# Performance work log

Hardware: AMD Instinct MI355X
Metric: run time of the kernel (lower is better)

## Reference

```python
import jax, jax.numpy as jnp
import numpy as np

N_LEVELS = 16
F = 2
LOG2_T = 19
T = 1 << LOG2_T
BASE_RES = 16.0
FINEST_RES = 512.0
N_SAMPLES = 128
NEAR, FAR = 2.0, 6.0
BOX_MIN = jnp.array([-1.5, -1.5, -1.5], jnp.float32)
BOX_MAX = jnp.array([1.5, 1.5, 1.5], jnp.float32)
GEO_FEAT = 15
OUT_CH = 4

_PRIMES = np.array([1, 2654435761, 805459861], dtype=np.uint32)
_OFFSETS = np.array([[i, j, k] for i in (0, 1) for j in (0, 1) for k in (0, 1)], dtype=np.int32)  # [8,3]
_B = np.exp((np.log(FINEST_RES) - np.log(BASE_RES)) / (N_LEVELS - 1))
_RESOLUTIONS = np.floor(BASE_RES * _B ** np.arange(N_LEVELS)).astype(np.float32)


def setup_inputs() -> dict:
    key = jax.random.key(0)
    ks = jax.random.split(key, 10)
    n_rays = 16384
    o = jax.random.uniform(ks[0], (n_rays, 3), jnp.float32, -0.5, 0.5)
    d = jax.random.normal(ks[1], (n_rays, 3), jnp.float32)
    d = d / jnp.linalg.norm(d, axis=-1, keepdims=True)
    rays = jnp.concatenate([o, d], -1)
    hash_tables = jax.random.uniform(ks[2], (N_LEVELS, T, F), jnp.float32, -1e-4, 1e-4)
    def w(k, di, do):
        return jax.random.normal(k, (di, do), jnp.float32) * (1.0 / np.sqrt(di))
    return dict(
        rays=rays,
        hash_tables=hash_tables,
        ws0=w(ks[3], 32, 64), ws1=w(ks[4], 64, 64), ws2=w(ks[5], 64, 1 + GEO_FEAT),
        wc0=w(ks[6], 16 + GEO_FEAT, 64), wc1=w(ks[7], 64, 64), wc2=w(ks[8], 64, 64), wc3=w(ks[9], 64, OUT_CH - 1),
    )


def _hash_embed(x, tables):
    """Multi-res hash grid: x [P,3] world coords, tables [L,T,F] -> ([P,L*F], keep_mask [P])."""
    xc = jnp.clip(x, BOX_MIN, BOX_MAX)
    keep = jnp.all(x == xc, axis=-1)
    offs = jnp.asarray(_OFFSETS)          # [8,3]
    primes = jnp.asarray(_PRIMES)         # uint32
    feats = []
    for l in range(N_LEVELS):
        grid = (BOX_MAX - BOX_MIN) / _RESOLUTIONS[l]
        bl = jnp.floor((xc - BOX_MIN) / grid).astype(jnp.int32)   # [P,3] bottom-left voxel index
        vmin = bl.astype(jnp.float32) * grid + BOX_MIN
        wts = (xc - vmin) / grid                                  # trilinear weights [P,3]
        corners = (bl[:, None, :] + offs[None]).astype(jnp.uint32)  # [P,8,3]
        h = (corners[..., 0] * primes[0]) ^ (corners[..., 1] * primes[1]) ^ (corners[..., 2] * primes[2])
        idx = (h & jnp.uint32(T - 1)).astype(jnp.int32)           # [P,8]
        e = tables[l][idx]                                        # [P,8,F]
        w0, w1, w2 = wts[:, 0:1], wts[:, 1:2], wts[:, 2:3]
        c00 = e[:, 0] * (1 - w0) + e[:, 4] * w0
        c01 = e[:, 1] * (1 - w0) + e[:, 5] * w0
        c10 = e[:, 2] * (1 - w0) + e[:, 6] * w0
        c11 = e[:, 3] * (1 - w0) + e[:, 7] * w0
        c0 = c00 * (1 - w1) + c10 * w1
        c1 = c01 * (1 - w1) + c11 * w1
        feats.append(c0 * (1 - w2) + c1 * w2)
    return jnp.concatenate(feats, -1), keep


def _sh_encode(d):
    """Degree-4 spherical harmonics encoding, [P,3] -> [P,16]."""
    x, y, z = d[..., 0], d[..., 1], d[..., 2]
    xx, yy, zz = x * x, y * y, z * z
    xy, yz, xz = x * y, y * z, x * z
    C0 = 0.28209479177387814
    C1 = 0.4886025119029199
    C2 = (1.0925484305920792, -1.0925484305920792, 0.31539156525252005, -1.0925484305920792, 0.5462742152960396)
    C3 = (-0.5900435899266435, 2.890611442640554, -0.4570457994644658, 0.3731763325901154,
          -0.4570457994644658, 1.445305721320277, -0.5900435899266435)
    return jnp.stack([
        jnp.full_like(x, C0),
        -C1 * y, C1 * z, -C1 * x,
        C2[0] * xy, C2[1] * yz, C2[2] * (2.0 * zz - xx - yy), C2[3] * xz, C2[4] * (xx - yy),
        C3[0] * y * (3.0 * xx - yy), C3[1] * xy * z, C3[2] * y * (4.0 * zz - xx - yy),
        C3[3] * z * (2.0 * zz - 3.0 * xx - 3.0 * yy), C3[4] * x * (4.0 * zz - xx - yy),
        C3[5] * z * (xx - yy), C3[6] * x * (xx - 3.0 * yy),
    ], axis=-1)


def _forward(rays, hash_tables, ws0, ws1, ws2, wc0, wc1, wc2, wc3):
    n_rays = rays.shape[0]
    o, d = rays[:, :3], rays[:, 3:6]
    z = jnp.linspace(NEAR, FAR, N_SAMPLES, dtype=jnp.float32)
    zvals = jnp.broadcast_to(z, (n_rays, N_SAMPLES))
    pts = o[:, None, :] + d[:, None, :] * z[None, :, None]       # [N,S,3]
    P = n_rays * N_SAMPLES
    pts_f = pts.reshape(P, 3)
    dirs_f = jnp.broadcast_to(d[:, None, :], (n_rays, N_SAMPLES, 3)).reshape(P, 3)

    enc_pts, keep = _hash_embed(pts_f, hash_tables)              # [P,32], [P]
    enc_dirs = _sh_encode(dirs_f)                                # [P,16]

    # NeRFSmall: bias-free sigma net then color net
    h = jnp.maximum(enc_pts @ ws0, 0.0)
    h = jnp.maximum(h @ ws1, 0.0)
    h = h @ ws2                                                   # [P, 1+GEO_FEAT]
    sigma, geo = h[:, 0], h[:, 1:]
    hc = jnp.concatenate([enc_dirs, geo], -1)
    hc = jnp.maximum(hc @ wc0, 0.0)
    hc = jnp.maximum(hc @ wc1, 0.0)
    hc = jnp.maximum(hc @ wc2, 0.0)
    color = hc @ wc3                                              # [P, OUT_CH-1]

    sigma = jnp.where(keep, sigma, 0.0)                           # output[~keep_mask, -1] = 0
    raw = jnp.concatenate([color, sigma[:, None]], -1).reshape(n_rays, N_SAMPLES, OUT_CH)

    # Integrator (raw2outputs)
    dists = zvals[:, 1:] - zvals[:, :-1]
    dists = jnp.concatenate([dists, jnp.full((n_rays, 1), 1e10, jnp.float32)], -1)
    dists = dists * jnp.linalg.norm(d, axis=-1, keepdims=True)
    chs = jax.nn.sigmoid(raw[..., :-1])
    alpha = 1.0 - jnp.exp(-jnp.maximum(raw[..., -1], 0.0) * dists)
    trans = jnp.cumprod(1.0 - alpha + 1e-10, axis=-1)
    trans = jnp.concatenate([jnp.ones((n_rays, 1), jnp.float32), trans[:, :-1]], -1)
    weights = alpha * trans
    chs_map = jnp.einsum('ns,nsc->nc', weights, chs)
    depth_map = jnp.sum(weights * zvals, -1)
    probs = jnp.concatenate([weights, 1.0 - jnp.sum(weights, -1, keepdims=True) + 1e-6], -1)
    p = probs / jnp.sum(probs, -1, keepdims=True)
    sparsity_loss = -jnp.sum(p * jnp.log(jnp.clip(p, 1e-37)), -1)
    return chs_map, depth_map, sparsity_loss


def reference(rays, hash_tables, ws0, ws1, ws2, wc0, wc1, wc2, wc3):
    return _forward(rays, hash_tables, ws0, ws1, ws2, wc0, wc1, wc2, wc3)
```

## Files before the change

kernel.cpp:

```cpp
#include <hip/hip_runtime.h>

#define NRAYS 16384
#define NLEV  16
#define THASH 524288
#define MAXACT 48
#define MAXPTS (NRAYS*MAXACT)
#define MBLK  512
#define MGRID 1024

__device__ __forceinline__ float zval32(int i) {
  const float step = 4.0f / 127.0f;
  return __fadd_rn(2.0f, __fmul_rn((float)i, step));
}
__device__ __forceinline__ float pcoord(float o, float d, float z) {
  return __fadd_rn(o, __fmul_rn(d, z));
}

__global__ __launch_bounds__(64)
void k_classify(const float* __restrict__ rays,
                float* __restrict__ sh,
                unsigned* __restrict__ counter,
                unsigned* __restrict__ rbase,
                unsigned* __restrict__ rn,
                unsigned* __restrict__ plist) {
  int r = blockIdx.x * 64 + threadIdx.x;
  if (r >= NRAYS) return;
  float ox = rays[6*r+0], oy = rays[6*r+1], oz = rays[6*r+2];
  float dx = rays[6*r+3], dy = rays[6*r+4], dz = rays[6*r+5];
  float x = dx, y = dy, z = dz;
  float xx = x*x, yy = y*y, zz = z*z, xy = x*y, yz = y*z, xz = x*z;
  float* shp = sh + 16*r;
  shp[0]  = 0.28209479177387814f;
  shp[1]  = -0.4886025119029199f * y;
  shp[2]  =  0.4886025119029199f * z;
  shp[3]  = -0.4886025119029199f * x;
  shp[4]  =  1.0925484305920792f * xy;
  shp[5]  = -1.0925484305920792f * yz;
  shp[6]  =  0.31539156525252005f * (2.0f*zz - xx - yy);
  shp[7]  = -1.0925484305920792f * xz;
  shp[8]  =  0.5462742152960396f * (xx - yy);
  shp[9]  = -0.5900435899266435f * y * (3.0f*xx - yy);
  shp[10] =  2.890611442640554f  * xy * z;
  shp[11] = -0.4570457994644658f * y * (4.0f*zz - xx - yy);
  shp[12] =  0.3731763325901154f * z * (2.0f*zz - 3.0f*xx - 3.0f*yy);
  shp[13] = -0.4570457994644658f * x * (4.0f*zz - xx - yy);
  shp[14] =  1.445305721320277f  * z * (xx - yy);
  shp[15] = -0.5900435899266435f * x * (xx - 3.0f*yy);
  int n = 0;
  for (int i = 0; i < 128; ++i) {
    float zi = zval32(i);
    float px = pcoord(ox, dx, zi);
    float py = pcoord(oy, dy, zi);
    float pz = pcoord(oz, dz, zi);
    bool in = (px >= -1.5f) && (px <= 1.5f) && (py >= -1.5f) && (py <= 1.5f)
           && (pz >= -1.5f) && (pz <= 1.5f);
    if (!in) break;
    ++n;
  }
  unsigned base = atomicAdd(counter, (unsigned)n);
  rbase[r] = base;
  rn[r]    = (unsigned)n;
  for (int i = 0; i < n; ++i) plist[base + i] = (unsigned)(r*128 + i);
}

template<int IN, int TOTOUT, int JC, bool RELU>
__device__ __forceinline__ void layer(const float* __restrict__ W, int jbase,
                                      const float* __restrict__ in,
                                      float* __restrict__ out, int lane) {
  float acc[JC];
#pragma unroll
  for (int j = 0; j < JC; ++j) acc[j] = 0.0f;
#pragma unroll 4
  for (int k = 0; k < IN; ++k) {
    float a = in[k*64 + lane];
    const float* Wk = W + k*TOTOUT + jbase;
#pragma unroll
    for (int j = 0; j < JC; ++j) acc[j] = fmaf(a, Wk[j], acc[j]);
  }
#pragma unroll
  for (int j = 0; j < JC; ++j)
    out[(jbase + j)*64 + lane] = RELU ? fmaxf(acc[j], 0.0f) : acc[j];
}

__global__ __launch_bounds__(MBLK)
void k_mlp(const float* __restrict__ rays,
           const float* __restrict__ tables,
           const float* __restrict__ w_s0, const float* __restrict__ w_s1,
           const float* __restrict__ w_s2, const float* __restrict__ w_c0,
           const float* __restrict__ w_c1, const float* __restrict__ w_c2,
           const float* __restrict__ w_c3,
           const float* __restrict__ sh,
           const unsigned* __restrict__ counter,
           const unsigned* __restrict__ plist,
           float4* __restrict__ results) {
  __shared__ float bufA[64*64];
  __shared__ float bufB[64*64];
  __shared__ float sig_s[64];
  __shared__ unsigned pid_s[64];
  const int t = threadIdx.x;
  const int lane = t & 63;
  const int q = __builtin_amdgcn_readfirstlane(t >> 6);
  const unsigned count = *counter;
  const unsigned ntiles = (count + 63u) >> 6;
  const float RESF[NLEV] = {16.f,20.f,25.f,32.f,40.f,50.f,64.f,80.f,
                            101.f,128.f,161.f,203.f,256.f,322.f,406.f,512.f};
  for (unsigned tile = blockIdx.x; tile < ntiles; tile += MGRID) {
    unsigned s0 = tile << 6;
    if (t < 64) {
      unsigned s = s0 + (unsigned)t;
      pid_s[t] = (s < count) ? plist[s] : 0u;
    }
    __syncthreads();
    {
      unsigned pid = pid_s[lane];
      int r = (int)(pid >> 7);
      int i = (int)(pid & 127u);
      float zi = zval32(i);
      float px = pcoord(rays[6*r+0], rays[6*r+3], zi);
      float py = pcoord(rays[6*r+1], rays[6*r+4], zi);
      float pz = pcoord(rays[6*r+2], rays[6*r+5], zi);
      float xcx = fminf(fmaxf(px, -1.5f), 1.5f);
      float xcy = fminf(fmaxf(py, -1.5f), 1.5f);
      float xcz = fminf(fmaxf(pz, -1.5f), 1.5f);
#pragma unroll
      for (int li = 0; li < 2; ++li) {
        int l = 2*q + li;
        const float grid = 3.0f / RESF[l];
        float bfx = floorf(__fdiv_rn(__fadd_rn(xcx, 1.5f), grid));
        float bfy = floorf(__fdiv_rn(__fadd_rn(xcy, 1.5f), grid));
        float bfz = floorf(__fdiv_rn(__fadd_rn(xcz, 1.5f), grid));
        float vmx = __fadd_rn(__fmul_rn(bfx, grid), -1.5f);
        float vmy = __fadd_rn(__fmul_rn(bfy, grid), -1.5f);
        float vmz = __fadd_rn(__fmul_rn(bfz, grid), -1.5f);
        float wx = __fdiv_rn(__fsub_rn(xcx, vmx), grid);
        float wy = __fdiv_rn(__fsub_rn(xcy, vmy), grid);
        float wz = __fdiv_rn(__fsub_rn(xcz, vmz), grid);
        unsigned cx0 = (unsigned)(int)bfx, cy0 = (unsigned)(int)bfy, cz0 = (unsigned)(int)bfz;
        unsigned cx1 = cx0 + 1u, cy1 = cy0 + 1u, cz1 = cz0 + 1u;
        unsigned hy0 = cy0*2654435761u, hy1 = cy1*2654435761u;
        unsigned hz0 = cz0*805459861u,  hz1 = cz1*805459861u;
        const float2* tb = (const float2*)tables + (size_t)l*THASH;
        float2 e000 = tb[(cx0^hy0^hz0)&(THASH-1)];
        float2 e001 = tb[(cx0^hy0^hz1)&(THASH-1)];
        float2 e010 = tb[(cx0^hy1^hz0)&(THASH-1)];
        float2 e011 = tb[(cx0^hy1^hz1)&(THASH-1)];
        float2 e100 = tb[(cx1^hy0^hz0)&(THASH-1)];
        float2 e101 = tb[(cx1^hy0^hz1)&(THASH-1)];
        float2 e110 = tb[(cx1^hy1^hz0)&(THASH-1)];
        float2 e111 = tb[(cx1^hy1^hz1)&(THASH-1)];
        float iwx = 1.f-wx, iwy = 1.f-wy, iwz = 1.f-wz;
        float c00a = e000.x*iwx + e100.x*wx, c00b = e000.y*iwx + e100.y*wx;
        float c01a = e001.x*iwx + e101.x*wx, c01b = e001.y*iwx + e101.y*wx;
        float c10a = e010.x*iwx + e110.x*wx, c10b = e010.y*iwx + e110.y*wx;
        float c11a = e011.x*iwx + e111.x*wx, c11b = e011.y*iwx + e111.y*wx;
        float c0a = c00a*iwy + c10a*wy, c0b = c00b*iwy + c10b*wy;
        float c1a = c01a*iwy + c11a*wy, c1b = c01b*iwy + c11b*wy;
        bufA[(2*l+0)*64 + lane] = c0a*iwz + c1a*wz;
        bufA[(2*l+1)*64 + lane] = c0b*iwz + c1b*wz;
      }
    }
    __syncthreads();
    layer<32,64,8,true >(w_s0, q*8, bufA, bufB, lane); __syncthreads();
    layer<64,64,8,true >(w_s1, q*8, bufB, bufA, lane); __syncthreads();
    layer<64,16,2,false>(w_s2, q*2, bufA, bufB, lane); __syncthreads();
    if (q == 0) sig_s[lane] = bufB[0*64 + lane];
    for (int idx = t; idx < 31*64; idx += MBLK) {
      int k = idx >> 6, p = idx & 63;
      float v;
      if (k < 16) v = sh[(pid_s[p] >> 7)*16 + k];
      else        v = bufB[(k-15)*64 + p];
      bufA[idx] = v;
    }
    __syncthreads();
    layer<31,64,8,true >(w_c0, q*8, bufA, bufB, lane); __syncthreads();
    layer<64,64,8,true >(w_c1, q*8, bufB, bufA, lane); __syncthreads();
    layer<64,64,8,true >(w_c2, q*8, bufA, bufB, lane); __syncthreads();
    if (q < 3) layer<64,3,1,false>(w_c3, q, bufB, bufA, lane);
    __syncthreads();
    if (q == 0) {
      unsigned s = s0 + (unsigned)lane;
      if (s < count) {
        float4 res;
        res.x = sig_s[lane];
        res.y = bufA[0*64 + lane];
        res.z = bufA[1*64 + lane];
        res.w = bufA[2*64 + lane];
        results[s] = res;
      }
    }
    __syncthreads();
  }
}

__global__ __launch_bounds__(64)
void k_comp(const float* __restrict__ rays,
            const unsigned* __restrict__ rbase,
            const unsigned* __restrict__ rn,
            const float4* __restrict__ results,
            float* __restrict__ out) {
  int r = blockIdx.x * 64 + threadIdx.x;
  if (r >= NRAYS) return;
  float dx = rays[6*r+3], dy = rays[6*r+4], dz = rays[6*r+5];
  float dnorm = sqrtf(dx*dx + dy*dy + dz*dz);
  int n = (int)rn[r];
  unsigned base = rbase[r];
  const float step = 4.0f/127.0f;
  const float diststep = __fmul_rn(step, dnorm);
  float S = 0.f, ch0 = 0.f, ch1 = 0.f, ch2 = 0.f, dep = 0.f, trans = 1.f;
  for (int i = 0; i < n; ++i) {
    float4 rs = results[base + i];
    float z = zval32(i);
    float sg = fmaxf(rs.x, 0.f);
    float alpha = -expm1f(-__fmul_rn(sg, diststep));
    float w = __fmul_rn(alpha, trans);
    trans = __fmul_rn(trans, __fadd_rn(__fsub_rn(1.f, alpha), 1e-10f));
    float s0 = 1.f/(1.f + expf(-rs.y));
    float s1 = 1.f/(1.f + expf(-rs.z));
    float s2 = 1.f/(1.f + expf(-rs.w));
    S += w; ch0 += w*s0; ch1 += w*s1; ch2 += w*s2; dep += w*z;
  }
  float rem  = __fadd_rn(__fsub_rn(1.f, S), 1e-6f);
  float Stot = __fadd_rn(S, rem);
  float loss = 0.f, trans2 = 1.f;
  for (int i = 0; i < n; ++i) {
    float4 rs = results[base + i];
    float sg = fmaxf(rs.x, 0.f);
    float alpha = -expm1f(-__fmul_rn(sg, diststep));
    float w = __fmul_rn(alpha, trans2);
    trans2 = __fmul_rn(trans2, __fadd_rn(__fsub_rn(1.f, alpha), 1e-10f));
    float p = __fdiv_rn(w, Stot);
    loss += p * logf(fmaxf(p, 1e-37f));
  }
  float pl = __fdiv_rn(rem, Stot);
  loss += pl * logf(fmaxf(pl, 1e-37f));
  out[3*r+0] = ch0; out[3*r+1] = ch1; out[3*r+2] = ch2;
  out[3*NRAYS + r] = dep;
  out[4*NRAYS + r] = -loss;
}

extern "C" void kernel_launch(void* const* d_in, const int* in_sizes, int n_in,
                              void* d_out, int out_size, void* d_ws, size_t ws_size,
                              hipStream_t stream) {
  const float* rays   = (const float*)d_in[0];
  const float* tables = (const float*)d_in[1];
  const float* ws0    = (const float*)d_in[2];
  const float* ws1    = (const float*)d_in[3];
  const float* ws2    = (const float*)d_in[4];
  const float* wc0    = (const float*)d_in[5];
  const float* wc1    = (const float*)d_in[6];
  const float* wc2    = (const float*)d_in[7];
  const float* wc3    = (const float*)d_in[8];

  char* ws = (char*)d_ws;
  unsigned* counter = (unsigned*)ws;
  unsigned* rbase   = (unsigned*)(ws + 256);
  unsigned* rn      = (unsigned*)(ws + 256 + 65536);
  float*    sh      = (float*)  (ws + 256 + 131072);
  float4*   results = (float4*) (ws + 1179904);
  unsigned* plist   = (unsigned*)(ws + 1179904 + (size_t)MAXPTS*16);

  hipMemsetAsync(counter, 0, 4, stream);
  k_classify<<<NRAYS/64, 64, 0, stream>>>(rays, sh, counter, rbase, rn, plist);
  k_mlp<<<MGRID, MBLK, 0, stream>>>(rays, tables, ws0, ws1, ws2,
                                    wc0, wc1, wc2, wc3, sh, counter, plist, results);
  k_comp<<<NRAYS/64, 64, 0, stream>>>(rays, rbase, rn, results, (float*)d_out);
}
```

Measured before the change: 185.4 us.

## Run MLP tile in a single wavefront per block and wave-aggregate classify atomics

The MLP kernel now uses one 64-thread wavefront per block. That wavefront computes all 16 hash levels itself and every layer with 64 accumulators per thread, so all __syncthreads barriers go away and each lane keeps a full point in registers. Classify replaces the per-thread atomicAdd with a wave prefix scan and a single atomic per wave. The trade is much higher register pressure (64 accumulators) and far fewer waves per CU, since each block still reserves 32KB of LDS. Latency hiding for the hash-table gathers is likely to get worse.

```diff
diff --git a/kernel.cpp b/kernel.cpp
--- a/kernel.cpp
+++ b/kernel.cpp
@@ -5,8 +5,7 @@
 #define THASH 524288
 #define MAXACT 48
 #define MAXPTS (NRAYS*MAXACT)
-#define MBLK  512
-#define MGRID 1024
+#define MGRID 2048
 
 __device__ __forceinline__ float zval32(int i) {
   const float step = 4.0f / 127.0f;
@@ -23,7 +22,8 @@
                 unsigned* __restrict__ rbase,
                 unsigned* __restrict__ rn,
                 unsigned* __restrict__ plist) {
-  int r = blockIdx.x * 64 + threadIdx.x;
+  int lane = threadIdx.x;
+  int r = blockIdx.x * 64 + lane;
   if (r >= NRAYS) return;
   float ox = rays[6*r+0], oy = rays[6*r+1], oz = rays[6*r+2];
   float dx = rays[6*r+3], dy = rays[6*r+4], dz = rays[6*r+5];
@@ -46,7 +46,7 @@
   shp[13] = -0.4570457994644658f * x * (4.0f*zz - xx - yy);
   shp[14] =  1.445305721320277f  * z * (xx - yy);
   shp[15] = -0.5900435899266435f * x * (xx - 3.0f*yy);
-  int n = 0;
+  unsigned n = 0;
   for (int i = 0; i < 128; ++i) {
     float zi = zval32(i);
     float px = pcoord(ox, dx, zi);
@@ -57,32 +57,43 @@
     if (!in) break;
     ++n;
   }
-  unsigned base = atomicAdd(counter, (unsigned)n);
+  unsigned pre = n;
+#pragma unroll
+  for (int d = 1; d < 64; d <<= 1) {
+    unsigned v = __shfl_up(pre, d, 64);
+    if (lane >= d) pre += v;
+  }
+  unsigned excl  = pre - n;
+  unsigned total = __shfl(pre, 63, 64);
+  unsigned base0 = 0;
+  if (lane == 0) base0 = atomicAdd(counter, total);
+  base0 = __shfl(base0, 0, 64);
+  unsigned base = base0 + excl;
   rbase[r] = base;
-  rn[r]    = (unsigned)n;
-  for (int i = 0; i < n; ++i) plist[base + i] = (unsigned)(r*128 + i);
-}
-
-template<int IN, int TOTOUT, int JC, bool RELU>
-__device__ __forceinline__ void layer(const float* __restrict__ W, int jbase,
-                                      const float* __restrict__ in,
-                                      float* __restrict__ out, int lane) {
-  float acc[JC];
-#pragma unroll
-  for (int j = 0; j < JC; ++j) acc[j] = 0.0f;
-#pragma unroll 4
+  rn[r]    = n;
+  for (unsigned i = 0; i < n; ++i) plist[base + i] = (unsigned)(r*128 + (int)i);
+}
+
+template<int IN, int TOTOUT, bool RELU>
+__device__ __forceinline__ void layerw(const float* __restrict__ W,
+                                       const float* __restrict__ in,
+                                       float* __restrict__ out, int lane) {
+  float acc[TOTOUT];
+#pragma unroll
+  for (int j = 0; j < TOTOUT; ++j) acc[j] = 0.0f;
+#pragma unroll 2
   for (int k = 0; k < IN; ++k) {
     float a = in[k*64 + lane];
-    const float* Wk = W + k*TOTOUT + jbase;
-#pragma unroll
-    for (int j = 0; j < JC; ++j) acc[j] = fmaf(a, Wk[j], acc[j]);
-  }
-#pragma unroll
-  for (int j = 0; j < JC; ++j)
-    out[(jbase + j)*64 + lane] = RELU ? fmaxf(acc[j], 0.0f) : acc[j];
-}
-
-__global__ __launch_bounds__(MBLK)
+    const float* Wk = W + k*TOTOUT;
+#pragma unroll
+    for (int j = 0; j < TOTOUT; ++j) acc[j] = fmaf(a, Wk[j], acc[j]);
+  }
+#pragma unroll
+  for (int j = 0; j < TOTOUT; ++j)
+    out[j*64 + lane] = RELU ? fmaxf(acc[j], 0.0f) : acc[j];
+}
+
+__global__ __launch_bounds__(64, 2)
 void k_mlp(const float* __restrict__ rays,
            const float* __restrict__ tables,
            const float* __restrict__ w_s0, const float* __restrict__ w_s1,
@@ -93,102 +104,86 @@
            const unsigned* __restrict__ counter,
            const unsigned* __restrict__ plist,
            float4* __restrict__ results) {
-  __shared__ float bufA[64*64];
-  __shared__ float bufB[64*64];
-  __shared__ float sig_s[64];
-  __shared__ unsigned pid_s[64];
-  const int t = threadIdx.x;
-  const int lane = t & 63;
-  const int q = __builtin_amdgcn_readfirstlane(t >> 6);
+  __shared__ float A[64*64];
+  __shared__ float B[64*64];
+  const int lane = threadIdx.x;
   const unsigned count = *counter;
   const unsigned ntiles = (count + 63u) >> 6;
   const float RESF[NLEV] = {16.f,20.f,25.f,32.f,40.f,50.f,64.f,80.f,
                             101.f,128.f,161.f,203.f,256.f,322.f,406.f,512.f};
   for (unsigned tile = blockIdx.x; tile < ntiles; tile += MGRID) {
-    unsigned s0 = tile << 6;
-    if (t < 64) {
-      unsigned s = s0 + (unsigned)t;
-      pid_s[t] = (s < count) ? plist[s] : 0u;
+    unsigned s = (tile << 6) + (unsigned)lane;
+    unsigned pid = (s < count) ? plist[s] : 0u;
+    int r = (int)(pid >> 7);
+    int i = (int)(pid & 127u);
+    float zi = zval32(i);
+    float px = pcoord(rays[6*r+0], rays[6*r+3], zi);
+    float py = pcoord(rays[6*r+1], rays[6*r+4], zi);
+    float pz = pcoord(rays[6*r+2], rays[6*r+5], zi);
+    float xcx = fminf(fmaxf(px, -1.5f), 1.5f);
+    float xcy = fminf(fmaxf(py, -1.5f), 1.5f);
+    float xcz = fminf(fmaxf(pz, -1.5f), 1.5f);
+#pragma unroll
+    for (int l = 0; l < NLEV; ++l) {
+      const float grid = 3.0f / RESF[l];
+      float bfx = floorf(__fdiv_rn(__fadd_rn(xcx, 1.5f), grid));
+      float bfy = floorf(__fdiv_rn(__fadd_rn(xcy, 1.5f), grid));
+      float bfz = floorf(__fdiv_rn(__fadd_rn(xcz, 1.5f), grid));
+      float vmx = __fadd_rn(__fmul_rn(bfx, grid), -1.5f);
+      float vmy = __fadd_rn(__fmul_rn(bfy, grid), -1.5f);
+      float vmz = __fadd_rn(__fmul_rn(bfz, grid), -1.5f);
+      float wx = __fdiv_rn(__fsub_rn(xcx, vmx), grid);
+      float wy = __fdiv_rn(__fsub_rn(xcy, vmy), grid);
+      float wz = __fdiv_rn(__fsub_rn(xcz, vmz), grid);
+      unsigned cx0 = (unsigned)(int)bfx, cy0 = (unsigned)(int)bfy, cz0 = (unsigned)(int)bfz;
+      unsigned cx1 = cx0 + 1u, cy1 = cy0 + 1u, cz1 = cz0 + 1u;
+      unsigned hy0 = cy0*2654435761u, hy1 = cy1*2654435761u;
+      unsigned hz0 = cz0*805459861u,  hz1 = cz1*805459861u;
+      const float2* tb = (const float2*)tables + (size_t)l*THASH;
+      float2 e000 = tb[(cx0^hy0^hz0)&(THASH-1)];
+      float2 e001 = tb[(cx0^hy0^hz1)&(THASH-1)];
+      float2 e010 = tb[(cx0^hy1^hz0)&(THASH-1)];
+      float2 e011 = tb[(cx0^hy1^hz1)&(THASH-1)];
+      float2 e100 = tb[(cx1^hy0^hz0)&(THASH-1)];
+      float2 e101 = tb[(cx1^hy0^hz1)&(THASH-1)];
+      float2 e110 = tb[(cx1^hy1^hz0)&(THASH-1)];
+      float2 e111 = tb[(cx1^hy1^hz1)&(THASH-1)];
+      float iwx = 1.f-wx, iwy = 1.f-wy, iwz = 1.f-wz;
+      float c00a = e000.x*iwx + e100.x*wx, c00b = e000.y*iwx + e100.y*wx;
+      float c01a = e001.x*iwx + e101.x*wx, c01b = e001.y*iwx + e101.y*wx;
+      float c10a = e010.x*iwx + e110.x*wx, c10b = e010.y*iwx + e110.y*wx;
+      float c11a = e011.x*iwx + e111.x*wx, c11b = e011.y*iwx + e111.y*wx;
+      float c0a = c00a*iwy + c10a*wy, c0b = c00b*iwy + c10b*wy;
+      float c1a = c01a*iwy + c11a*wy, c1b = c01b*iwy + c11b*wy;
+      A[(2*l+0)*64 + lane] = c0a*iwz + c1a*wz;
+      A[(2*l+1)*64 + lane] = c0b*iwz + c1b*wz;
     }
-    __syncthreads();
+    layerw<32,64,true >(w_s0, A, B, lane);
+    layerw<64,64,true >(w_s1, B, A, lane);
+    layerw<64,16,false>(w_s2, A, B, lane);
+    float sigma = B[0*64 + lane];
     {
-      unsigned pid = pid_s[lane];
-      int r = (int)(pid >> 7);
-      int i = (int)(pid & 127u);
-      float zi = zval32(i);
-      float px = pcoord(rays[6*r+0], rays[6*r+3], zi);
-      float py = pcoord(rays[6*r+1], rays[6*r+4], zi);
-      float pz = pcoord(rays[6*r+2], rays[6*r+5], zi);
-      float xcx = fminf(fmaxf(px, -1.5f), 1.5f);
-      float xcy = fminf(fmaxf(py, -1.5f), 1.5f);
-      float xcz = fminf(fmaxf(pz, -1.5f), 1.5f);
-#pragma unroll
-      for (int li = 0; li < 2; ++li) {
-        int l = 2*q + li;
-        const float grid = 3.0f / RESF[l];
-        float bfx = floorf(__fdiv_rn(__fadd_rn(xcx, 1.5f), grid));
-        float bfy = floorf(__fdiv_rn(__fadd_rn(xcy, 1.5f), grid));
-        float bfz = floorf(__fdiv_rn(__fadd_rn(xcz, 1.5f), grid));
-        float vmx = __fadd_rn(__fmul_rn(bfx, grid), -1.5f);
-        float vmy = __fadd_rn(__fmul_rn(bfy, grid), -1.5f);
-        float vmz = __fadd_rn(__fmul_rn(bfz, grid), -1.5f);
-        float wx = __fdiv_rn(__fsub_rn(xcx, vmx), grid);
-        float wy = __fdiv_rn(__fsub_rn(xcy, vmy), grid);
-        float wz = __fdiv_rn(__fsub_rn(xcz, vmz), grid);
-        unsigned cx0 = (unsigned)(int)bfx, cy0 = (unsigned)(int)bfy, cz0 = (unsigned)(int)bfz;
-        unsigned cx1 = cx0 + 1u, cy1 = cy0 + 1u, cz1 = cz0 + 1u;
-        unsigned hy0 = cy0*2654435761u, hy1 = cy1*2654435761u;
-        unsigned hz0 = cz0*805459861u,  hz1 = cz1*805459861u;
-        const float2* tb = (const float2*)tables + (size_t)l*THASH;
-        float2 e000 = tb[(cx0^hy0^hz0)&(THASH-1)];
-        float2 e001 = tb[(cx0^hy0^hz1)&(THASH-1)];
-        float2 e010 = tb[(cx0^hy1^hz0)&(THASH-1)];
-        float2 e011 = tb[(cx0^hy1^hz1)&(THASH-1)];
-        float2 e100 = tb[(cx1^hy0^hz0)&(THASH-1)];
-        float2 e101 = tb[(cx1^hy0^hz1)&(THASH-1)];
-        float2 e110 = tb[(cx1^hy1^hz0)&(THASH-1)];
-        float2 e111 = tb[(cx1^hy1^hz1)&(THASH-1)];
-        float iwx = 1.f-wx, iwy = 1.f-wy, iwz = 1.f-wz;
-        float c00a = e000.x*iwx + e100.x*wx, c00b = e000.y*iwx + e100.y*wx;
-        float c01a = e001.x*iwx + e101.x*wx, c01b = e001.y*iwx + e101.y*wx;
-        float c10a = e010.x*iwx + e110.x*wx, c10b = e010.y*iwx + e110.y*wx;
-        float c11a = e011.x*iwx + e111.x*wx, c11b = e011.y*iwx + e111.y*wx;
-        float c0a = c00a*iwy + c10a*wy, c0b = c00b*iwy + c10b*wy;
-        float c1a = c01a*iwy + c11a*wy, c1b = c01b*iwy + c11b*wy;
-        bufA[(2*l+0)*64 + lane] = c0a*iwz + c1a*wz;
-        bufA[(2*l+1)*64 + lane] = c0b*iwz + c1b*wz;
-      }
+      const float4* sh4 = (const float4*)(sh + 16*r);
+      float4 v0 = sh4[0], v1 = sh4[1], v2 = sh4[2], v3 = sh4[3];
+      A[ 0*64+lane]=v0.x; A[ 1*64+lane]=v0.y; A[ 2*64+lane]=v0.z; A[ 3*64+lane]=v0.w;
+      A[ 4*64+lane]=v1.x; A[ 5*64+lane]=v1.y; A[ 6*64+lane]=v1.z; A[ 7*64+lane]=v1.w;
+      A[ 8*64+lane]=v2.x; A[ 9*64+lane]=v2.y; A[10*64+lane]=v2.z; A[11*64+lane]=v2.w;
+      A[12*64+lane]=v3.x; A[13*64+lane]=v3.y; A[14*64+lane]=v3.z; A[15*64+lane]=v3.w;
+#pragma unroll
+      for (int m = 0; m < 15; ++m) A[(16+m)*64 + lane] = B[(1+m)*64 + lane];
     }
-    __syncthreads();
-    layer<32,64,8,true >(w_s0, q*8, bufA, bufB, lane); __syncthreads();
-    layer<64,64,8,true >(w_s1, q*8, bufB, bufA, lane); __syncthreads();
-    layer<64,16,2,false>(w_s2, q*2, bufA, bufB, lane); __syncthreads();
-    if (q == 0) sig_s[lane] = bufB[0*64 + lane];
-    for (int idx = t; idx < 31*64; idx += MBLK) {
-      int k = idx >> 6, p = idx & 63;
-      float v;
-      if (k < 16) v = sh[(pid_s[p] >> 7)*16 + k];
-      else        v = bufB[(k-15)*64 + p];
-      bufA[idx] = v;
+    layerw<31,64,true >(w_c0, A, B, lane);
+    layerw<64,64,true >(w_c1, B, A, lane);
+    layerw<64,64,true >(w_c2, A, B, lane);
+    layerw<64, 3,false>(w_c3, B, A, lane);
+    if (s < count) {
+      float4 res;
+      res.x = sigma;
+      res.y = A[0*64 + lane];
+      res.z = A[1*64 + lane];
+      res.w = A[2*64 + lane];
+      results[s] = res;
     }
-    __syncthreads();
-    layer<31,64,8,true >(w_c0, q*8, bufA, bufB, lane); __syncthreads();
-    layer<64,64,8,true >(w_c1, q*8, bufB, bufA, lane); __syncthreads();
-    layer<64,64,8,true >(w_c2, q*8, bufA, bufB, lane); __syncthreads();
-    if (q < 3) layer<64,3,1,false>(w_c3, q, bufB, bufA, lane);
-    __syncthreads();
-    if (q == 0) {
-      unsigned s = s0 + (unsigned)lane;
-      if (s < count) {
-        float4 res;
-        res.x = sig_s[lane];
-        res.y = bufA[0*64 + lane];
-        res.z = bufA[1*64 + lane];
-        res.w = bufA[2*64 + lane];
-        results[s] = res;
-      }
-    }
-    __syncthreads();
   }
 }
 
@@ -261,7 +256,7 @@
 
   hipMemsetAsync(counter, 0, 4, stream);
   k_classify<<<NRAYS/64, 64, 0, stream>>>(rays, sh, counter, rbase, rn, plist);
-  k_mlp<<<MGRID, MBLK, 0, stream>>>(rays, tables, ws0, ws1, ws2,
-                                    wc0, wc1, wc2, wc3, sh, counter, plist, results);
+  k_mlp<<<MGRID, 64, 0, stream>>>(rays, tables, ws0, ws1, ws2,
+                                  wc0, wc1, wc2, wc3, sh, counter, plist, results);
   k_comp<<<NRAYS/64, 64, 0, stream>>>(rays, rbase, rn, results, (float*)d_out);
 }
```

New measurement: 401.9 us. 117% more time.
